# Kernel tuning notes

Hardware: AMD Instinct MI355X
Metric: run time of the kernel (lower is better)

## Reference

```python
import jax, jax.numpy as jnp
import numpy as np

NSQ = 3  # lstm_num_square


def setup_inputs() -> dict:
    key = jax.random.key(0)
    k1, k2, k3, k4, k5 = jax.random.split(key, 5)
    B, C, T, H = 64, 2, 128, 96
    blk = H // NSQ
    V = blk * blk  # downsample.version = 1024
    x = jax.random.normal(k1, (B, C, T, H, H), dtype=jnp.float32)
    # Per-block LSTM params, hidden_size=1, gate order (i, f, g, o) as in PyTorch.
    # PyTorch init: uniform(-1/sqrt(hidden), 1/sqrt(hidden)) = uniform(-1, 1) here.
    W_ih = jax.random.uniform(k2, (NSQ, NSQ, 4, V), minval=-1.0, maxval=1.0, dtype=jnp.float32)
    W_hh = jax.random.uniform(k3, (NSQ, NSQ, 4), minval=-1.0, maxval=1.0, dtype=jnp.float32)
    b_ih = jax.random.uniform(k4, (NSQ, NSQ, 4), minval=-1.0, maxval=1.0, dtype=jnp.float32)
    b_hh = jax.random.uniform(k5, (NSQ, NSQ, 4), minval=-1.0, maxval=1.0, dtype=jnp.float32)
    return {"x": x, "W_ih": W_ih, "W_hh": W_hh, "b_ih": b_ih, "b_hh": b_hh}


def reference(x, W_ih, W_hh, b_ih, b_hh):
    # x: (B, C, T, H, H); only channel 0 is used (as in the original module).
    B, _, T, H, _ = x.shape
    blk = H // NSQ
    V = blk * blk
    # Downsample: split HxH grid into NSQ x NSQ blocks, flatten each block.
    xs = x[:, 0].reshape(B, T, NSQ, blk, NSQ, blk)
    xs = xs.transpose(1, 0, 2, 4, 3, 5).reshape(T, B, NSQ, NSQ, V)  # (T,B,n,n,V)
    # Precompute input contributions to all 4 gates for all blocks at once.
    x_gates = jnp.einsum('tbijv,ijgv->tbijg', xs, W_ih) + b_ih + b_hh  # (T,B,n,n,4)

    def step(carry, xg):
        h, c = carry  # each (B, n, n), hidden_size = 1 per block
        g = xg + W_hh * h[..., None]  # (B,n,n,4)
        i = jax.nn.sigmoid(g[..., 0])
        f = jax.nn.sigmoid(g[..., 1])
        gg = jnp.tanh(g[..., 2])
        o = jax.nn.sigmoid(g[..., 3])
        c = f * c + i * gg
        h = o * jnp.tanh(c)
        return (h, c), h

    h0 = jnp.zeros((B, NSQ, NSQ), dtype=x.dtype)
    c0 = jnp.zeros((B, NSQ, NSQ), dtype=x.dtype)
    _, hs = jax.lax.scan(step, (h0, c0), x_gates)
    return hs  # (T, B, NSQ, NSQ)
```

## Files before the change

kernel.cpp:

```cpp
#include <hip/hip_runtime.h>

#define T_LEN 128
#define B_SZ  64
#define NC    9
#define H_SZ  96
#define V_SZ  1024
#define MT    8

__global__ __launch_bounds__(256) void gates_kernel(
    const float* __restrict__ x,
    const float* __restrict__ W_ih,
    float* __restrict__ xg)
{
    const int lane  = threadIdx.x & 63;
    const int wid   = threadIdx.x >> 6;
    const int wave  = blockIdx.x * 4 + wid;
    const int cell  = wave >> 10;
    const int chunk = wave & 1023;
    const int i = cell / 3, j = cell % 3;

    float4 wf[4][4];
    const float* wbase = W_ih + (size_t)cell * 4 * V_SZ;
    #pragma unroll
    for (int k = 0; k < 4; ++k) {
        const int v = k * 256 + lane * 4;
        #pragma unroll
        for (int g = 0; g < 4; ++g)
            wf[k][g] = *(const float4*)(wbase + g * V_SZ + v);
    }

    const int p0 = lane >> 3;
    const int q0 = (lane & 7) * 4;
    const int colbase = j * 32 + q0;

    const int tb0 = chunk * MT;
    #pragma unroll 2
    for (int m = 0; m < MT; ++m) {
        const int tb = tb0 + m;
        const int t  = tb >> 6;
        const int b  = tb & 63;
        const float* slab = x + ((size_t)(b * 2) * T_LEN + t) * (H_SZ * H_SZ);

        float a0 = 0.f, a1 = 0.f, a2 = 0.f, a3 = 0.f;
        #pragma unroll
        for (int k = 0; k < 4; ++k) {
            const int p = k * 8 + p0;
            const float4 xv = *(const float4*)(slab + (i * 32 + p) * H_SZ + colbase);
            a0 = fmaf(xv.x, wf[k][0].x, fmaf(xv.y, wf[k][0].y, fmaf(xv.z, wf[k][0].z, fmaf(xv.w, wf[k][0].w, a0))));
            a1 = fmaf(xv.x, wf[k][1].x, fmaf(xv.y, wf[k][1].y, fmaf(xv.z, wf[k][1].z, fmaf(xv.w, wf[k][1].w, a1))));
            a2 = fmaf(xv.x, wf[k][2].x, fmaf(xv.y, wf[k][2].y, fmaf(xv.z, wf[k][2].z, fmaf(xv.w, wf[k][2].w, a2))));
            a3 = fmaf(xv.x, wf[k][3].x, fmaf(xv.y, wf[k][3].y, fmaf(xv.z, wf[k][3].z, fmaf(xv.w, wf[k][3].w, a3))));
        }

        #pragma unroll
        for (int off = 32; off; off >>= 1) {
            a0 += __shfl_xor(a0, off, 64);
            a1 += __shfl_xor(a1, off, 64);
            a2 += __shfl_xor(a2, off, 64);
            a3 += __shfl_xor(a3, off, 64);
        }

        if (lane == 0) {
            float4 r = make_float4(a0, a1, a2, a3);
            *(float4*)(xg + ((size_t)tb * NC + cell) * 4) = r;
        }
    }
}

__global__ __launch_bounds__(64) void scan_kernel(
    const float* __restrict__ xg,
    const float* __restrict__ W_hh,
    const float* __restrict__ b_ih,
    const float* __restrict__ b_hh,
    float* __restrict__ out)
{
    const int tid  = blockIdx.x * 64 + threadIdx.x;
    const int cell = tid % 9;

    const float4 wh = *(const float4*)(W_hh + cell * 4);
    const float4 bi = *(const float4*)(b_ih + cell * 4);
    const float4 bh = *(const float4*)(b_hh + cell * 4);
    const float bx = bi.x + bh.x, by = bi.y + bh.y, bz = bi.z + bh.z, bw = bi.w + bh.w;

    const float4* xg4 = (const float4*)xg;

    float h = 0.f, c = 0.f;
    float4 g = xg4[tid];
    for (int t = 0; t < T_LEN; ++t) {
        const int tn = (t + 1 < T_LEN) ? t + 1 : t;
        const float4 gn = xg4[(size_t)tn * (B_SZ * NC) + tid];

        const float gi = g.x + bx + wh.x * h;
        const float gf = g.y + by + wh.y * h;
        const float gz = g.z + bz + wh.z * h;
        const float go = g.w + bw + wh.w * h;

        const float ii = 1.f / (1.f + __expf(-gi));
        const float ff = 1.f / (1.f + __expf(-gf));
        const float gt = tanhf(gz);
        const float oo = 1.f / (1.f + __expf(-go));

        c = ff * c + ii * gt;
        h = oo * tanhf(c);

        out[(size_t)t * (B_SZ * NC) + tid] = h;
        g = gn;
    }
}

extern "C" void kernel_launch(void* const* d_in, const int* in_sizes, int n_in,
                              void* d_out, int out_size, void* d_ws, size_t ws_size,
                              hipStream_t stream) {
    const float* x    = (const float*)d_in[0];
    const float* W_ih = (const float*)d_in[1];
    const float* W_hh = (const float*)d_in[2];
    const float* b_ih = (const float*)d_in[3];
    const float* b_hh = (const float*)d_in[4];
    float* out = (float*)d_out;

    float* xg = (float*)d_ws;

    gates_kernel<<<dim3((NC * (T_LEN * B_SZ / MT)) / 4), dim3(256), 0, stream>>>(x, W_ih, xg);

    scan_kernel<<<dim3(NC), dim3(64), 0, stream>>>(xg, W_hh, b_ih, b_hh, out);
}
```

Before: 759.4 us.

## Prefetch next x tile, use transpose-reduce for gates, and fast LSTM activations

The gates kernel now loads the next time-batch slab into registers while computing the current one, so global load latency overlaps with the FMAs. The four per-gate wave reductions become a butterfly transpose-reduce that needs fewer shuffles, and each of the first four lanes writes one gate value. The scan kernel swaps IEEE division and tanhf for hardware reciprocal plus exp based sigmoid and tanh, which shortens the serial recurrence at some cost in accuracy. Register pressure goes up from the prefetch buffers.

```diff
diff --git a/kernel.cpp b/kernel.cpp
--- a/kernel.cpp
+++ b/kernel.cpp
@@ -31,40 +31,67 @@
 
     const int p0 = lane >> 3;
     const int q0 = (lane & 7) * 4;
-    const int colbase = j * 32 + q0;
+    const int rowcol = (i * 32) * H_SZ + j * 32 + q0;
 
     const int tb0 = chunk * MT;
-    #pragma unroll 2
+
+    float4 xv[4];
+    {
+        const int t = tb0 >> 6, b = tb0 & 63;
+        const float* slab = x + ((size_t)(b * 2) * T_LEN + t) * (H_SZ * H_SZ) + rowcol;
+        #pragma unroll
+        for (int k = 0; k < 4; ++k)
+            xv[k] = *(const float4*)(slab + (k * 8 + p0) * H_SZ);
+    }
+
+    #pragma unroll
     for (int m = 0; m < MT; ++m) {
-        const int tb = tb0 + m;
-        const int t  = tb >> 6;
-        const int b  = tb & 63;
-        const float* slab = x + ((size_t)(b * 2) * T_LEN + t) * (H_SZ * H_SZ);
+        float4 nx[4];
+        if (m + 1 < MT) {
+            const int tbn = tb0 + m + 1;
+            const int t = tbn >> 6, b = tbn & 63;
+            const float* slab = x + ((size_t)(b * 2) * T_LEN + t) * (H_SZ * H_SZ) + rowcol;
+            #pragma unroll
+            for (int k = 0; k < 4; ++k)
+                nx[k] = *(const float4*)(slab + (k * 8 + p0) * H_SZ);
+        }
 
         float a0 = 0.f, a1 = 0.f, a2 = 0.f, a3 = 0.f;
         #pragma unroll
         for (int k = 0; k < 4; ++k) {
-            const int p = k * 8 + p0;
-            const float4 xv = *(const float4*)(slab + (i * 32 + p) * H_SZ + colbase);
-            a0 = fmaf(xv.x, wf[k][0].x, fmaf(xv.y, wf[k][0].y, fmaf(xv.z, wf[k][0].z, fmaf(xv.w, wf[k][0].w, a0))));
-            a1 = fmaf(xv.x, wf[k][1].x, fmaf(xv.y, wf[k][1].y, fmaf(xv.z, wf[k][1].z, fmaf(xv.w, wf[k][1].w, a1))));
-            a2 = fmaf(xv.x, wf[k][2].x, fmaf(xv.y, wf[k][2].y, fmaf(xv.z, wf[k][2].z, fmaf(xv.w, wf[k][2].w, a2))));
-            a3 = fmaf(xv.x, wf[k][3].x, fmaf(xv.y, wf[k][3].y, fmaf(xv.z, wf[k][3].z, fmaf(xv.w, wf[k][3].w, a3))));
+            const float4 v = xv[k];
+            a0 = fmaf(v.x, wf[k][0].x, fmaf(v.y, wf[k][0].y, fmaf(v.z, wf[k][0].z, fmaf(v.w, wf[k][0].w, a0))));
+            a1 = fmaf(v.x, wf[k][1].x, fmaf(v.y, wf[k][1].y, fmaf(v.z, wf[k][1].z, fmaf(v.w, wf[k][1].w, a1))));
+            a2 = fmaf(v.x, wf[k][2].x, fmaf(v.y, wf[k][2].y, fmaf(v.z, wf[k][2].z, fmaf(v.w, wf[k][2].w, a2))));
+            a3 = fmaf(v.x, wf[k][3].x, fmaf(v.y, wf[k][3].y, fmaf(v.z, wf[k][3].z, fmaf(v.w, wf[k][3].w, a3))));
         }
 
+        const bool m1 = (lane & 1) != 0;
+        float y01 = m1 ? a0 : a1;
+        float a01 = (m1 ? a1 : a0) + __shfl_xor(y01, 1, 64);
+        float y23 = m1 ? a2 : a3;
+        float a23 = (m1 ? a3 : a2) + __shfl_xor(y23, 1, 64);
+        const bool m2 = (lane & 2) != 0;
+        float ys = m2 ? a01 : a23;
+        float s  = (m2 ? a23 : a01) + __shfl_xor(ys, 2, 64);
+        s += __shfl_xor(s, 4, 64);
+        s += __shfl_xor(s, 8, 64);
+        s += __shfl_xor(s, 16, 64);
+        s += __shfl_xor(s, 32, 64);
+
+        if (lane < 4)
+            xg[((size_t)(tb0 + m) * NC + cell) * 4 + lane] = s;
+
         #pragma unroll
-        for (int off = 32; off; off >>= 1) {
-            a0 += __shfl_xor(a0, off, 64);
-            a1 += __shfl_xor(a1, off, 64);
-            a2 += __shfl_xor(a2, off, 64);
-            a3 += __shfl_xor(a3, off, 64);
-        }
+        for (int k = 0; k < 4; ++k) xv[k] = nx[k];
+    }
+}
 
-        if (lane == 0) {
-            float4 r = make_float4(a0, a1, a2, a3);
-            *(float4*)(xg + ((size_t)tb * NC + cell) * 4) = r;
-        }
-    }
+__device__ __forceinline__ float fsig(float xx) {
+    return __builtin_amdgcn_rcpf(1.f + __expf(-xx));
+}
+__device__ __forceinline__ float ftanh(float xx) {
+    return fmaf(-2.f, __builtin_amdgcn_rcpf(1.f + __expf(2.f * xx)), 1.f);
 }
 
 __global__ __launch_bounds__(64) void scan_kernel(
@@ -90,18 +117,18 @@
         const int tn = (t + 1 < T_LEN) ? t + 1 : t;
         const float4 gn = xg4[(size_t)tn * (B_SZ * NC) + tid];
 
-        const float gi = g.x + bx + wh.x * h;
-        const float gf = g.y + by + wh.y * h;
-        const float gz = g.z + bz + wh.z * h;
-        const float go = g.w + bw + wh.w * h;
+        const float gi = fmaf(wh.x, h, g.x + bx);
+        const float gf = fmaf(wh.y, h, g.y + by);
+        const float gz = fmaf(wh.z, h, g.z + bz);
+        const float go = fmaf(wh.w, h, g.w + bw);
 
-        const float ii = 1.f / (1.f + __expf(-gi));
-        const float ff = 1.f / (1.f + __expf(-gf));
-        const float gt = tanhf(gz);
-        const float oo = 1.f / (1.f + __expf(-go));
+        const float ii = fsig(gi);
+        const float ff = fsig(gf);
+        const float gt = ftanh(gz);
+        const float oo = fsig(go);
 
-        c = ff * c + ii * gt;
-        h = oo * tanhf(c);
+        c = fmaf(ff, c, ii * gt);
+        h = oo * ftanh(c);
 
         out[(size_t)t * (B_SZ * NC) + tid] = h;
         g = gn;
@@ -121,6 +148,5 @@
     float* xg = (float*)d_ws;
 
     gates_kernel<<<dim3((NC * (T_LEN * B_SZ / MT)) / 4), dim3(256), 0, stream>>>(x, W_ih, xg);
-
     scan_kernel<<<dim3(NC), dim3(64), 0, stream>>>(xg, W_hh, b_ih, b_hh, out);
 }
```

New measurement: 733.7 us. 1.04x faster.
